# Performance work log

Measured on AMD Instinct MI355X. Metric: run time of the kernel, lower is better.

## Reference

```python
import jax, jax.numpy as jnp
import numpy as np

WINDOW_SIZE = 11
N_CHANNELS = 3
SIGMA = 1.5
K1, K2 = 0.01, 0.03
VALUE_RANGE = 1.0


def _create_window(window_size: int, n_channels: int, sigma: float) -> np.ndarray:
    # 1D gaussian, normalized, then outer product -> 2D kernel
    coords = np.arange(window_size, dtype=np.float32) - (window_size - 1) / 2.0
    g = np.exp(-(coords ** 2) / (2.0 * sigma ** 2))
    g = g / g.sum()
    k2d = np.outer(g, g).astype(np.float32)  # (K, K), sums to 1
    # depthwise kernel, OIHW with I=1 (groups = n_channels)
    return np.broadcast_to(k2d, (n_channels, 1, window_size, window_size)).copy()


def _dwconv(x, window):
    # depthwise valid conv, NCHW / OIHW
    return jax.lax.conv_general_dilated(
        x, window, window_strides=(1, 1), padding='VALID',
        feature_group_count=window.shape[0],
        dimension_numbers=('NCHW', 'OIHW', 'NCHW'))


def setup_inputs() -> dict:
    key = jax.random.key(0)
    kx, ky = jax.random.split(key)
    N, C, H, W = 32, N_CHANNELS, 512, 512
    x = jax.random.uniform(kx, (N, C, H, W), dtype=jnp.float32)
    y = jax.random.uniform(ky, (N, C, H, W), dtype=jnp.float32)
    window = jnp.asarray(_create_window(WINDOW_SIZE, N_CHANNELS, SIGMA))
    return {"x": x, "y": y, "window": window}


def reference(x, y, window):
    c1 = (K1 * VALUE_RANGE) ** 2
    c2 = (K2 * VALUE_RANGE) ** 2

    mu_x = _dwconv(x, window)
    mu_y = _dwconv(y, window)
    mu_x_sq = mu_x ** 2
    mu_y_sq = mu_y ** 2
    mu_xy = mu_x * mu_y

    sigma_x_sq = _dwconv(x * x, window) - mu_x_sq
    sigma_y_sq = _dwconv(y * y, window) - mu_y_sq
    sigma_xy = _dwconv(x * y, window) - mu_xy

    cs = (2.0 * sigma_xy + c2) / (sigma_x_sq + sigma_y_sq + c2)
    ss = (2.0 * mu_xy + c1) / (mu_x_sq + mu_y_sq + c1) * cs

    l = ss.mean(axis=(-1, -2))  # (N, C) per-channel SSIM
    l = l.mean(axis=-1)         # (N,)  per-sample
    return l.mean()             # reduction='mean'
```

## Files before the change

kernel.cpp:

```cpp
#include <hip/hip_runtime.h>

#define KS     11
#define HH     512
#define WW     512
#define OUTD   502
#define OH     45
#define ROWS   55
#define NBANDS 12
#define NSTRIP 4
#define SCOLS  128
#define LCOLS  140
#define NIMG   96
#define NACC   256

__global__ __launch_bounds__(64, 2)
void ssim_main(const float* __restrict__ xg, const float* __restrict__ yg,
               const float* __restrict__ win, double* __restrict__ acc_out,
               const int accmask)
{
    __shared__ float shs[2][LCOLS];
    __shared__ float shd[2][LCOLS];

    const int tid   = threadIdx.x;
    const int bid   = blockIdx.x;
    const int strip = bid & (NSTRIP - 1);
    const int band  = (bid >> 2) % NBANDS;
    const int img   = bid / (NSTRIP * NBANDS);
    const int row0  = band * OH;
    const int colb  = strip * SCOLS;
    const int c0    = colb + 2 * tid;
    const int l0    = 2 * tid;

    float g[6];
    #pragma unroll
    for (int i = 0; i < 6; i++) {
        float s = 0.f;
        #pragma unroll
        for (int j = 0; j < KS; j++) s += win[i * KS + j];
        g[i] = s;
    }
#define G(j) g[(j) <= 5 ? (j) : 10 - (j)]

    const float* xi = xg + (size_t)img * (HH * WW);
    const float* yi = yg + (size_t)img * (HH * WW);

    const bool hn = (tid < (LCOLS - SCOLS) / 2);
    int hcol = colb + SCOLS + 2 * tid;
    if (hcol > WW - 2) hcol = WW - 2;

    float acc[4][2][KS];
    #pragma unroll
    for (int q = 0; q < 4; q++)
        #pragma unroll
        for (int c = 0; c < 2; c++)
            #pragma unroll
            for (int s = 0; s < KS; s++) acc[q][c][s] = 0.f;

    float ssum = 0.f;
    const float C1x2 = 0.0002f;
    const float C2x2 = 0.0018f;

    float2 pfs, pfd, phs, phd;
    {
        int gr = row0;
        float2 ax = *(const float2*)&xi[gr * WW + c0];
        float2 ay = *(const float2*)&yi[gr * WW + c0];
        shs[0][l0] = ax.x + ay.x; shs[0][l0 + 1] = ax.y + ay.y;
        shd[0][l0] = ax.x - ay.x; shd[0][l0 + 1] = ax.y - ay.y;
        if (hn) {
            float2 bx = *(const float2*)&xi[gr * WW + hcol];
            float2 by = *(const float2*)&yi[gr * WW + hcol];
            shs[0][SCOLS + l0] = bx.x + by.x; shs[0][SCOLS + l0 + 1] = bx.y + by.y;
            shd[0][SCOLS + l0] = bx.x - by.x; shd[0][SCOLS + l0 + 1] = bx.y - by.y;
        }
        gr = row0 + 1;
        ax = *(const float2*)&xi[gr * WW + c0];
        ay = *(const float2*)&yi[gr * WW + c0];
        pfs = make_float2(ax.x + ay.x, ax.y + ay.y);
        pfd = make_float2(ax.x - ay.x, ax.y - ay.y);
        phs = make_float2(0.f, 0.f); phd = make_float2(0.f, 0.f);
        if (hn) {
            float2 bx = *(const float2*)&xi[gr * WW + hcol];
            float2 by = *(const float2*)&yi[gr * WW + hcol];
            phs = make_float2(bx.x + by.x, bx.y + by.y);
            phd = make_float2(bx.x - by.x, bx.y - by.y);
        }
    }

    #pragma unroll 1
    for (int rb = 0; rb < ROWS / KS; rb++) {
        #pragma unroll
        for (int rr = 0; rr < KS; rr++) {
            const int r = rb * KS + rr;

            const float* sb = shs[r & 1];
            const float* db = shd[r & 1];
            float sv[12], dv[12];
            #pragma unroll
            for (int k = 0; k < 6; k++) {
                float2 a = *(const float2*)&sb[l0 + 2 * k];
                float2 b = *(const float2*)&db[l0 + 2 * k];
                sv[2 * k] = a.x; sv[2 * k + 1] = a.y;
                dv[2 * k] = b.x; dv[2 * k + 1] = b.y;
            }

            if (r + 1 < ROWS) {
                float* sw = shs[(r + 1) & 1];
                float* dw = shd[(r + 1) & 1];
                sw[l0] = pfs.x; sw[l0 + 1] = pfs.y;
                dw[l0] = pfd.x; dw[l0 + 1] = pfd.y;
                if (hn) {
                    sw[SCOLS + l0] = phs.x; sw[SCOLS + l0 + 1] = phs.y;
                    dw[SCOLS + l0] = phd.x; dw[SCOLS + l0 + 1] = phd.y;
                }
            }
            if (r + 2 < ROWS) {
                int gr = row0 + r + 2; if (gr > HH - 1) gr = HH - 1;
                float2 ax = *(const float2*)&xi[gr * WW + c0];
                float2 ay = *(const float2*)&yi[gr * WW + c0];
                pfs = make_float2(ax.x + ay.x, ax.y + ay.y);
                pfd = make_float2(ax.x - ay.x, ax.y - ay.y);
                if (hn) {
                    float2 bx = *(const float2*)&xi[gr * WW + hcol];
                    float2 by = *(const float2*)&yi[gr * WW + hcol];
                    phs = make_float2(bx.x + by.x, bx.y + by.y);
                    phd = make_float2(bx.x - by.x, bx.y - by.y);
                }
            }

            float h0a = 0.f, h0b = 0.f, h1a = 0.f, h1b = 0.f;
            float h2a = 0.f, h2b = 0.f, h3a = 0.f, h3b = 0.f;
            float ts = sv[0] * sv[0];
            float td = dv[0] * dv[0];
            #pragma unroll
            for (int j = 0; j < KS; j++) {
                const float gj  = G(j);
                const float tsn = sv[j + 1] * sv[j + 1];
                const float tdn = dv[j + 1] * dv[j + 1];
                h0a = fmaf(gj, sv[j],     h0a); h0b = fmaf(gj, sv[j + 1], h0b);
                h1a = fmaf(gj, dv[j],     h1a); h1b = fmaf(gj, dv[j + 1], h1b);
                h2a = fmaf(gj, ts,        h2a); h2b = fmaf(gj, tsn,       h2b);
                h3a = fmaf(gj, td,        h3a); h3b = fmaf(gj, tdn,       h3b);
                ts = tsn; td = tdn;
            }

            {
                const float g0 = G(0);
                acc[0][0][rr] = g0 * h0a; acc[0][1][rr] = g0 * h0b;
                acc[1][0][rr] = g0 * h1a; acc[1][1][rr] = g0 * h1b;
                acc[2][0][rr] = g0 * h2a; acc[2][1][rr] = g0 * h2b;
                acc[3][0][rr] = g0 * h3a; acc[3][1][rr] = g0 * h3b;
            }
            #pragma unroll
            for (int i = 1; i < KS; i++) {
                const int slot = (rr - i + KS) % KS;
                const float gi = G(i);
                acc[0][0][slot] = fmaf(gi, h0a, acc[0][0][slot]);
                acc[0][1][slot] = fmaf(gi, h0b, acc[0][1][slot]);
                acc[1][0][slot] = fmaf(gi, h1a, acc[1][0][slot]);
                acc[1][1][slot] = fmaf(gi, h1b, acc[1][1][slot]);
                acc[2][0][slot] = fmaf(gi, h2a, acc[2][0][slot]);
                acc[2][1][slot] = fmaf(gi, h2b, acc[2][1][slot]);
                acc[3][0][slot] = fmaf(gi, h3a, acc[3][0][slot]);
                acc[3][1][slot] = fmaf(gi, h3b, acc[3][1][slot]);
            }

            const int es   = (rr + 1) % KS;
            const int jloc = r - (KS - 1);
            if (jloc >= 0 && jloc < OH && (row0 + jloc) < OUTD) {
                #pragma unroll
                for (int c = 0; c < 2; c++) {
                    if (c0 + c < OUTD) {
                        const float ms = acc[0][c][es], md = acc[1][c][es];
                        const float Ss = acc[2][c][es], Sd = acc[3][c][es];
                        const float a = ms * ms, b = md * md;
                        const float P = a - b;
                        const float Q = a + b;
                        const float U = Ss - Sd;
                        const float V = Ss + Sd;
                        const float num = (P + C1x2) * ((U - P) + C2x2);
                        const float den = (Q + C1x2) * ((V - Q) + C2x2);
                        float rc = __builtin_amdgcn_rcpf(den);
                        rc = rc * fmaf(-den, rc, 2.0f);
                        ssum = fmaf(num, rc, ssum);
                    }
                }
            }
        }
    }

    #pragma unroll
    for (int off = 32; off > 0; off >>= 1)
        ssum += __shfl_down(ssum, off);
    if (tid == 0)
        atomicAdd(&acc_out[bid & accmask], (double)ssum);
}

__global__ void ssim_finalize(const double* __restrict__ acc, float* __restrict__ out,
                              const int nacc)
{
    double s = 0.0;
    for (int i = threadIdx.x; i < nacc; i += 64) s += acc[i];
    #pragma unroll
    for (int off = 32; off > 0; off >>= 1)
        s += __shfl_down(s, off);
    if (threadIdx.x == 0)
        out[0] = (float)(s * (1.0 / 24192384.0));
}

extern "C" void kernel_launch(void* const* d_in, const int* in_sizes, int n_in,
                              void* d_out, int out_size, void* d_ws, size_t ws_size,
                              hipStream_t stream)
{
    const float* x   = (const float*)d_in[0];
    const float* y   = (const float*)d_in[1];
    const float* win = (const float*)d_in[2];
    float* out = (float*)d_out;
    double* acc = (double*)d_ws;

    const int nacc = (ws_size >= NACC * sizeof(double)) ? NACC : 1;
    hipMemsetAsync(acc, 0, nacc * sizeof(double), stream);
    ssim_main<<<dim3(NIMG * NBANDS * NSTRIP), dim3(64), 0, stream>>>(
        x, y, win, acc, nacc - 1);
    ssim_finalize<<<dim3(1), dim3(64), 0, stream>>>(acc, out, nacc);
}
```

Before: 329.4 us.

## Replace LDS row buffer with wavefront shuffles and interleaved x/y lanes

Each wavefront now covers a 52-column strip. Lanes alternate between loading x and y pairs, and each lane pair builds sum and difference values through xor shuffles. The horizontal 11-tap window is gathered with shuffle-down, so the shared-memory double buffer and its staging stores go away. Bands grow taller (133 output rows), which shrinks the vertical halo overhead, and register state is halved so launch bounds can allow 4 waves per SIMD. The cost is redundant halo columns per strip (64 lanes for 52 outputs), many extra cross-lane shuffles per row, and fewer blocks in total.

```diff
diff --git a/kernel.cpp b/kernel.cpp
--- a/kernel.cpp
+++ b/kernel.cpp
@@ -4,32 +4,26 @@
 #define HH     512
 #define WW     512
 #define OUTD   502
-#define OH     45
-#define ROWS   55
-#define NBANDS 12
-#define NSTRIP 4
-#define SCOLS  128
-#define LCOLS  140
+#define OH     133
+#define ROWS   143
+#define NBANDS 4
+#define ECOLS  52
+#define NSTRIP 10
 #define NIMG   96
 #define NACC   256
 
-__global__ __launch_bounds__(64, 2)
+__global__ __launch_bounds__(64, 4)
 void ssim_main(const float* __restrict__ xg, const float* __restrict__ yg,
                const float* __restrict__ win, double* __restrict__ acc_out,
                const int accmask)
 {
-    __shared__ float shs[2][LCOLS];
-    __shared__ float shd[2][LCOLS];
-
-    const int tid   = threadIdx.x;
-    const int bid   = blockIdx.x;
-    const int strip = bid & (NSTRIP - 1);
-    const int band  = (bid >> 2) % NBANDS;
-    const int img   = bid / (NSTRIP * NBANDS);
-    const int row0  = band * OH;
-    const int colb  = strip * SCOLS;
-    const int c0    = colb + 2 * tid;
-    const int l0    = 2 * tid;
+    const int lane   = threadIdx.x;
+    const int bid    = blockIdx.x;
+    const int strip  = bid % NSTRIP;
+    const int band   = (bid / NSTRIP) % NBANDS;
+    const int img    = bid / (NSTRIP * NBANDS);
+    const int row0   = band * OH;
+    const int parity = lane & 1;
 
     float g[6];
     #pragma unroll
@@ -41,16 +35,14 @@
     }
 #define G(j) g[(j) <= 5 ? (j) : 10 - (j)]
 
-    const float* xi = xg + (size_t)img * (HH * WW);
-    const float* yi = yg + (size_t)img * (HH * WW);
+    int gcol = ECOLS * strip + (lane & ~1);
+    if (gcol > WW - 2) gcol = WW - 2;
+    const float* srcp = (parity ? yg : xg) + (size_t)img * (HH * WW) + gcol;
+    const float sgn = parity ? -1.f : 1.f;
 
-    const bool hn = (tid < (LCOLS - SCOLS) / 2);
-    int hcol = colb + SCOLS + 2 * tid;
-    if (hcol > WW - 2) hcol = WW - 2;
-
-    float acc[4][2][KS];
+    float acc[2][2][KS];
     #pragma unroll
-    for (int q = 0; q < 4; q++)
+    for (int q = 0; q < 2; q++)
         #pragma unroll
         for (int c = 0; c < 2; c++)
             #pragma unroll
@@ -60,32 +52,7 @@
     const float C1x2 = 0.0002f;
     const float C2x2 = 0.0018f;
 
-    float2 pfs, pfd, phs, phd;
-    {
-        int gr = row0;
-        float2 ax = *(const float2*)&xi[gr * WW + c0];
-        float2 ay = *(const float2*)&yi[gr * WW + c0];
-        shs[0][l0] = ax.x + ay.x; shs[0][l0 + 1] = ax.y + ay.y;
-        shd[0][l0] = ax.x - ay.x; shd[0][l0 + 1] = ax.y - ay.y;
-        if (hn) {
-            float2 bx = *(const float2*)&xi[gr * WW + hcol];
-            float2 by = *(const float2*)&yi[gr * WW + hcol];
-            shs[0][SCOLS + l0] = bx.x + by.x; shs[0][SCOLS + l0 + 1] = bx.y + by.y;
-            shd[0][SCOLS + l0] = bx.x - by.x; shd[0][SCOLS + l0 + 1] = bx.y - by.y;
-        }
-        gr = row0 + 1;
-        ax = *(const float2*)&xi[gr * WW + c0];
-        ay = *(const float2*)&yi[gr * WW + c0];
-        pfs = make_float2(ax.x + ay.x, ax.y + ay.y);
-        pfd = make_float2(ax.x - ay.x, ax.y - ay.y);
-        phs = make_float2(0.f, 0.f); phd = make_float2(0.f, 0.f);
-        if (hn) {
-            float2 bx = *(const float2*)&xi[gr * WW + hcol];
-            float2 by = *(const float2*)&yi[gr * WW + hcol];
-            phs = make_float2(bx.x + by.x, bx.y + by.y);
-            phd = make_float2(bx.x - by.x, bx.y - by.y);
-        }
-    }
+    float2 pf = *(const float2*)(srcp + (size_t)row0 * WW);
 
     #pragma unroll 1
     for (int rb = 0; rb < ROWS / KS; rb++) {
@@ -93,98 +60,76 @@
         for (int rr = 0; rr < KS; rr++) {
             const int r = rb * KS + rr;
 
-            const float* sb = shs[r & 1];
-            const float* db = shd[r & 1];
-            float sv[12], dv[12];
-            #pragma unroll
-            for (int k = 0; k < 6; k++) {
-                float2 a = *(const float2*)&sb[l0 + 2 * k];
-                float2 b = *(const float2*)&db[l0 + 2 * k];
-                sv[2 * k] = a.x; sv[2 * k + 1] = a.y;
-                dv[2 * k] = b.x; dv[2 * k + 1] = b.y;
+            const float2 cur = pf;
+            {
+                int gr = row0 + r + 1; if (gr > HH - 1) gr = HH - 1;
+                pf = *(const float2*)(srcp + (size_t)gr * WW);
             }
 
-            if (r + 1 < ROWS) {
-                float* sw = shs[(r + 1) & 1];
-                float* dw = shd[(r + 1) & 1];
-                sw[l0] = pfs.x; sw[l0 + 1] = pfs.y;
-                dw[l0] = pfd.x; dw[l0 + 1] = pfd.y;
-                if (hn) {
-                    sw[SCOLS + l0] = phs.x; sw[SCOLS + l0 + 1] = phs.y;
-                    dw[SCOLS + l0] = phd.x; dw[SCOLS + l0 + 1] = phd.y;
-                }
-            }
-            if (r + 2 < ROWS) {
-                int gr = row0 + r + 2; if (gr > HH - 1) gr = HH - 1;
-                float2 ax = *(const float2*)&xi[gr * WW + c0];
-                float2 ay = *(const float2*)&yi[gr * WW + c0];
-                pfs = make_float2(ax.x + ay.x, ax.y + ay.y);
-                pfd = make_float2(ax.x - ay.x, ax.y - ay.y);
-                if (hn) {
-                    float2 bx = *(const float2*)&xi[gr * WW + hcol];
-                    float2 by = *(const float2*)&yi[gr * WW + hcol];
-                    phs = make_float2(bx.x + by.x, bx.y + by.y);
-                    phd = make_float2(bx.x - by.x, bx.y - by.y);
-                }
+            const float px = __shfl_xor(cur.x, 1);
+            const float py = __shfl_xor(cur.y, 1);
+            const float v0 = fmaf(sgn, cur.x, px);
+            const float v1 = fmaf(sgn, cur.y, py);
+
+            float sv[12];
+            sv[0] = v0; sv[1] = v1;
+            #pragma unroll
+            for (int k = 1; k <= 5; k++) {
+                sv[2 * k]     = __shfl_down(v0, 2 * k);
+                sv[2 * k + 1] = __shfl_down(v1, 2 * k);
             }
 
-            float h0a = 0.f, h0b = 0.f, h1a = 0.f, h1b = 0.f;
-            float h2a = 0.f, h2b = 0.f, h3a = 0.f, h3b = 0.f;
-            float ts = sv[0] * sv[0];
-            float td = dv[0] * dv[0];
+            float hv0 = 0.f, hv1 = 0.f, hq0 = 0.f, hq1 = 0.f;
+            float q0 = sv[0] * sv[0];
             #pragma unroll
             for (int j = 0; j < KS; j++) {
-                const float gj  = G(j);
-                const float tsn = sv[j + 1] * sv[j + 1];
-                const float tdn = dv[j + 1] * dv[j + 1];
-                h0a = fmaf(gj, sv[j],     h0a); h0b = fmaf(gj, sv[j + 1], h0b);
-                h1a = fmaf(gj, dv[j],     h1a); h1b = fmaf(gj, dv[j + 1], h1b);
-                h2a = fmaf(gj, ts,        h2a); h2b = fmaf(gj, tsn,       h2b);
-                h3a = fmaf(gj, td,        h3a); h3b = fmaf(gj, tdn,       h3b);
-                ts = tsn; td = tdn;
+                const float gj = G(j);
+                const float q1 = sv[j + 1] * sv[j + 1];
+                hv0 = fmaf(gj, sv[j],     hv0);
+                hv1 = fmaf(gj, sv[j + 1], hv1);
+                hq0 = fmaf(gj, q0,        hq0);
+                hq1 = fmaf(gj, q1,        hq1);
+                q0 = q1;
             }
 
             {
                 const float g0 = G(0);
-                acc[0][0][rr] = g0 * h0a; acc[0][1][rr] = g0 * h0b;
-                acc[1][0][rr] = g0 * h1a; acc[1][1][rr] = g0 * h1b;
-                acc[2][0][rr] = g0 * h2a; acc[2][1][rr] = g0 * h2b;
-                acc[3][0][rr] = g0 * h3a; acc[3][1][rr] = g0 * h3b;
+                acc[0][0][rr] = g0 * hv0; acc[0][1][rr] = g0 * hv1;
+                acc[1][0][rr] = g0 * hq0; acc[1][1][rr] = g0 * hq1;
             }
             #pragma unroll
             for (int i = 1; i < KS; i++) {
                 const int slot = (rr - i + KS) % KS;
                 const float gi = G(i);
-                acc[0][0][slot] = fmaf(gi, h0a, acc[0][0][slot]);
-                acc[0][1][slot] = fmaf(gi, h0b, acc[0][1][slot]);
-                acc[1][0][slot] = fmaf(gi, h1a, acc[1][0][slot]);
-                acc[1][1][slot] = fmaf(gi, h1b, acc[1][1][slot]);
-                acc[2][0][slot] = fmaf(gi, h2a, acc[2][0][slot]);
-                acc[2][1][slot] = fmaf(gi, h2b, acc[2][1][slot]);
-                acc[3][0][slot] = fmaf(gi, h3a, acc[3][0][slot]);
-                acc[3][1][slot] = fmaf(gi, h3b, acc[3][1][slot]);
+                acc[0][0][slot] = fmaf(gi, hv0, acc[0][0][slot]);
+                acc[0][1][slot] = fmaf(gi, hv1, acc[0][1][slot]);
+                acc[1][0][slot] = fmaf(gi, hq0, acc[1][0][slot]);
+                acc[1][1][slot] = fmaf(gi, hq1, acc[1][1][slot]);
             }
 
             const int es   = (rr + 1) % KS;
             const int jloc = r - (KS - 1);
-            if (jloc >= 0 && jloc < OH && (row0 + jloc) < OUTD) {
-                #pragma unroll
-                for (int c = 0; c < 2; c++) {
-                    if (c0 + c < OUTD) {
-                        const float ms = acc[0][c][es], md = acc[1][c][es];
-                        const float Ss = acc[2][c][es], Sd = acc[3][c][es];
-                        const float a = ms * ms, b = md * md;
-                        const float P = a - b;
-                        const float Q = a + b;
-                        const float U = Ss - Sd;
-                        const float V = Ss + Sd;
-                        const float num = (P + C1x2) * ((U - P) + C2x2);
-                        const float den = (Q + C1x2) * ((V - Q) + C2x2);
-                        float rc = __builtin_amdgcn_rcpf(den);
-                        rc = rc * fmaf(-den, rc, 2.0f);
-                        ssum = fmaf(num, rc, ssum);
-                    }
-                }
+            const int ecol = ECOLS * strip + lane;
+            if (jloc >= 0 && jloc < OH && (row0 + jloc) < OUTD &&
+                lane < ECOLS && ecol < OUTD) {
+                const float pm0 = __shfl_xor(acc[0][0][es], 1);
+                const float pm1 = __shfl_xor(acc[0][1][es], 1);
+                const float pS0 = __shfl_xor(acc[1][0][es], 1);
+                const float pS1 = __shfl_xor(acc[1][1][es], 1);
+                const float ms = parity ? pm1 : acc[0][0][es];
+                const float md = parity ? acc[0][1][es] : pm0;
+                const float Ss = parity ? pS1 : acc[1][0][es];
+                const float Sd = parity ? acc[1][1][es] : pS0;
+                const float a = ms * ms, b = md * md;
+                const float P = a - b;
+                const float Q = a + b;
+                const float U = Ss - Sd;
+                const float V = Ss + Sd;
+                const float num = (P + C1x2) * ((U - P) + C2x2);
+                const float den = (Q + C1x2) * ((V - Q) + C2x2);
+                float rc = __builtin_amdgcn_rcpf(den);
+                rc = rc * fmaf(-den, rc, 2.0f);
+                ssum = fmaf(num, rc, ssum);
             }
         }
     }
@@ -192,7 +137,7 @@
     #pragma unroll
     for (int off = 32; off > 0; off >>= 1)
         ssum += __shfl_down(ssum, off);
-    if (tid == 0)
+    if (lane == 0)
         atomicAdd(&acc_out[bid & accmask], (double)ssum);
 }
 
```

Measured after the change: 274.1 us. 16.8% less time.

## Load overlapping row windows directly from global memory instead of via LDS, taller bands

Applied to the files above, without the earlier changes.

Each lane now loads its own 12-column window of x and y straight from global memory, six float2 loads per input per row, and keeps the sums and differences in registers. This drops the shared-memory double buffer and its writes and reads. Band height grows from 45 to 67 output rows, with 8 bands instead of 12, which cuts the fraction of halo rows that get recomputed. In exchange, each lane issues six times as many global/L1 loads per row, grid size drops by a third, and register pressure rises from the larger prefetch arrays.

```diff
diff --git a/kernel.cpp b/kernel.cpp
--- a/kernel.cpp
+++ b/kernel.cpp
@@ -4,12 +4,11 @@
 #define HH     512
 #define WW     512
 #define OUTD   502
-#define OH     45
-#define ROWS   55
-#define NBANDS 12
+#define OH     67
+#define ROWS   77
+#define NBANDS 8
+#define SCOLS  128
 #define NSTRIP 4
-#define SCOLS  128
-#define LCOLS  140
 #define NIMG   96
 #define NACC   256
 
@@ -18,18 +17,13 @@
                const float* __restrict__ win, double* __restrict__ acc_out,
                const int accmask)
 {
-    __shared__ float shs[2][LCOLS];
-    __shared__ float shd[2][LCOLS];
-
-    const int tid   = threadIdx.x;
+    const int lane  = threadIdx.x;
     const int bid   = blockIdx.x;
     const int strip = bid & (NSTRIP - 1);
     const int band  = (bid >> 2) % NBANDS;
     const int img   = bid / (NSTRIP * NBANDS);
     const int row0  = band * OH;
-    const int colb  = strip * SCOLS;
-    const int c0    = colb + 2 * tid;
-    const int l0    = 2 * tid;
+    const int bc    = strip * SCOLS + 2 * lane;
 
     float g[6];
     #pragma unroll
@@ -41,12 +35,15 @@
     }
 #define G(j) g[(j) <= 5 ? (j) : 10 - (j)]
 
+    int coff[6];
+    #pragma unroll
+    for (int k = 0; k < 6; k++) {
+        int c = bc + 2 * k;
+        coff[k] = (c > WW - 2) ? (WW - 2) : c;
+    }
+
     const float* xi = xg + (size_t)img * (HH * WW);
     const float* yi = yg + (size_t)img * (HH * WW);
-
-    const bool hn = (tid < (LCOLS - SCOLS) / 2);
-    int hcol = colb + SCOLS + 2 * tid;
-    if (hcol > WW - 2) hcol = WW - 2;
 
     float acc[4][2][KS];
     #pragma unroll
@@ -60,30 +57,25 @@
     const float C1x2 = 0.0002f;
     const float C2x2 = 0.0018f;
 
-    float2 pfs, pfd, phs, phd;
+    float sv[12], dv[12];
+    float2 lx[6], ly[6];
+
     {
-        int gr = row0;
-        float2 ax = *(const float2*)&xi[gr * WW + c0];
-        float2 ay = *(const float2*)&yi[gr * WW + c0];
-        shs[0][l0] = ax.x + ay.x; shs[0][l0 + 1] = ax.y + ay.y;
-        shd[0][l0] = ax.x - ay.x; shd[0][l0 + 1] = ax.y - ay.y;
-        if (hn) {
-            float2 bx = *(const float2*)&xi[gr * WW + hcol];
-            float2 by = *(const float2*)&yi[gr * WW + hcol];
-            shs[0][SCOLS + l0] = bx.x + by.x; shs[0][SCOLS + l0 + 1] = bx.y + by.y;
-            shd[0][SCOLS + l0] = bx.x - by.x; shd[0][SCOLS + l0 + 1] = bx.y - by.y;
+        const float* xr = xi + (size_t)row0 * WW;
+        const float* yr = yi + (size_t)row0 * WW;
+        #pragma unroll
+        for (int k = 0; k < 6; k++) {
+            float2 a = *(const float2*)(xr + coff[k]);
+            float2 b = *(const float2*)(yr + coff[k]);
+            sv[2 * k] = a.x + b.x; sv[2 * k + 1] = a.y + b.y;
+            dv[2 * k] = a.x - b.x; dv[2 * k + 1] = a.y - b.y;
         }
-        gr = row0 + 1;
-        ax = *(const float2*)&xi[gr * WW + c0];
-        ay = *(const float2*)&yi[gr * WW + c0];
-        pfs = make_float2(ax.x + ay.x, ax.y + ay.y);
-        pfd = make_float2(ax.x - ay.x, ax.y - ay.y);
-        phs = make_float2(0.f, 0.f); phd = make_float2(0.f, 0.f);
-        if (hn) {
-            float2 bx = *(const float2*)&xi[gr * WW + hcol];
-            float2 by = *(const float2*)&yi[gr * WW + hcol];
-            phs = make_float2(bx.x + by.x, bx.y + by.y);
-            phd = make_float2(bx.x - by.x, bx.y - by.y);
+        const float* xr1 = xi + (size_t)(row0 + 1) * WW;
+        const float* yr1 = yi + (size_t)(row0 + 1) * WW;
+        #pragma unroll
+        for (int k = 0; k < 6; k++) {
+            lx[k] = *(const float2*)(xr1 + coff[k]);
+            ly[k] = *(const float2*)(yr1 + coff[k]);
         }
     }
 
@@ -93,76 +85,41 @@
         for (int rr = 0; rr < KS; rr++) {
             const int r = rb * KS + rr;
 
-            const float* sb = shs[r & 1];
-            const float* db = shd[r & 1];
-            float sv[12], dv[12];
-            #pragma unroll
-            for (int k = 0; k < 6; k++) {
-                float2 a = *(const float2*)&sb[l0 + 2 * k];
-                float2 b = *(const float2*)&db[l0 + 2 * k];
-                sv[2 * k] = a.x; sv[2 * k + 1] = a.y;
-                dv[2 * k] = b.x; dv[2 * k + 1] = b.y;
-            }
-
-            if (r + 1 < ROWS) {
-                float* sw = shs[(r + 1) & 1];
-                float* dw = shd[(r + 1) & 1];
-                sw[l0] = pfs.x; sw[l0 + 1] = pfs.y;
-                dw[l0] = pfd.x; dw[l0 + 1] = pfd.y;
-                if (hn) {
-                    sw[SCOLS + l0] = phs.x; sw[SCOLS + l0 + 1] = phs.y;
-                    dw[SCOLS + l0] = phd.x; dw[SCOLS + l0 + 1] = phd.y;
-                }
-            }
-            if (r + 2 < ROWS) {
-                int gr = row0 + r + 2; if (gr > HH - 1) gr = HH - 1;
-                float2 ax = *(const float2*)&xi[gr * WW + c0];
-                float2 ay = *(const float2*)&yi[gr * WW + c0];
-                pfs = make_float2(ax.x + ay.x, ax.y + ay.y);
-                pfd = make_float2(ax.x - ay.x, ax.y - ay.y);
-                if (hn) {
-                    float2 bx = *(const float2*)&xi[gr * WW + hcol];
-                    float2 by = *(const float2*)&yi[gr * WW + hcol];
-                    phs = make_float2(bx.x + by.x, bx.y + by.y);
-                    phd = make_float2(bx.x - by.x, bx.y - by.y);
-                }
-            }
-
-            float h0a = 0.f, h0b = 0.f, h1a = 0.f, h1b = 0.f;
-            float h2a = 0.f, h2b = 0.f, h3a = 0.f, h3b = 0.f;
-            float ts = sv[0] * sv[0];
-            float td = dv[0] * dv[0];
+            float hs0 = 0.f, hs1 = 0.f, hd0 = 0.f, hd1 = 0.f;
+            float hS0 = 0.f, hS1 = 0.f, hD0 = 0.f, hD1 = 0.f;
+            float qs = sv[0] * sv[0];
+            float qd = dv[0] * dv[0];
             #pragma unroll
             for (int j = 0; j < KS; j++) {
                 const float gj  = G(j);
-                const float tsn = sv[j + 1] * sv[j + 1];
-                const float tdn = dv[j + 1] * dv[j + 1];
-                h0a = fmaf(gj, sv[j],     h0a); h0b = fmaf(gj, sv[j + 1], h0b);
-                h1a = fmaf(gj, dv[j],     h1a); h1b = fmaf(gj, dv[j + 1], h1b);
-                h2a = fmaf(gj, ts,        h2a); h2b = fmaf(gj, tsn,       h2b);
-                h3a = fmaf(gj, td,        h3a); h3b = fmaf(gj, tdn,       h3b);
-                ts = tsn; td = tdn;
+                const float qs1 = sv[j + 1] * sv[j + 1];
+                const float qd1 = dv[j + 1] * dv[j + 1];
+                hs0 = fmaf(gj, sv[j],     hs0);  hs1 = fmaf(gj, sv[j + 1], hs1);
+                hd0 = fmaf(gj, dv[j],     hd0);  hd1 = fmaf(gj, dv[j + 1], hd1);
+                hS0 = fmaf(gj, qs,        hS0);  hS1 = fmaf(gj, qs1,       hS1);
+                hD0 = fmaf(gj, qd,        hD0);  hD1 = fmaf(gj, qd1,       hD1);
+                qs = qs1; qd = qd1;
             }
 
             {
                 const float g0 = G(0);
-                acc[0][0][rr] = g0 * h0a; acc[0][1][rr] = g0 * h0b;
-                acc[1][0][rr] = g0 * h1a; acc[1][1][rr] = g0 * h1b;
-                acc[2][0][rr] = g0 * h2a; acc[2][1][rr] = g0 * h2b;
-                acc[3][0][rr] = g0 * h3a; acc[3][1][rr] = g0 * h3b;
+                acc[0][0][rr] = g0 * hs0; acc[0][1][rr] = g0 * hs1;
+                acc[1][0][rr] = g0 * hd0; acc[1][1][rr] = g0 * hd1;
+                acc[2][0][rr] = g0 * hS0; acc[2][1][rr] = g0 * hS1;
+                acc[3][0][rr] = g0 * hD0; acc[3][1][rr] = g0 * hD1;
             }
             #pragma unroll
             for (int i = 1; i < KS; i++) {
                 const int slot = (rr - i + KS) % KS;
                 const float gi = G(i);
-                acc[0][0][slot] = fmaf(gi, h0a, acc[0][0][slot]);
-                acc[0][1][slot] = fmaf(gi, h0b, acc[0][1][slot]);
-                acc[1][0][slot] = fmaf(gi, h1a, acc[1][0][slot]);
-                acc[1][1][slot] = fmaf(gi, h1b, acc[1][1][slot]);
-                acc[2][0][slot] = fmaf(gi, h2a, acc[2][0][slot]);
-                acc[2][1][slot] = fmaf(gi, h2b, acc[2][1][slot]);
-                acc[3][0][slot] = fmaf(gi, h3a, acc[3][0][slot]);
-                acc[3][1][slot] = fmaf(gi, h3b, acc[3][1][slot]);
+                acc[0][0][slot] = fmaf(gi, hs0, acc[0][0][slot]);
+                acc[0][1][slot] = fmaf(gi, hs1, acc[0][1][slot]);
+                acc[1][0][slot] = fmaf(gi, hd0, acc[1][0][slot]);
+                acc[1][1][slot] = fmaf(gi, hd1, acc[1][1][slot]);
+                acc[2][0][slot] = fmaf(gi, hS0, acc[2][0][slot]);
+                acc[2][1][slot] = fmaf(gi, hS1, acc[2][1][slot]);
+                acc[3][0][slot] = fmaf(gi, hD0, acc[3][0][slot]);
+                acc[3][1][slot] = fmaf(gi, hD1, acc[3][1][slot]);
             }
 
             const int es   = (rr + 1) % KS;
@@ -170,7 +127,7 @@
             if (jloc >= 0 && jloc < OH && (row0 + jloc) < OUTD) {
                 #pragma unroll
                 for (int c = 0; c < 2; c++) {
-                    if (c0 + c < OUTD) {
+                    if (bc + c < OUTD) {
                         const float ms = acc[0][c][es], md = acc[1][c][es];
                         const float Ss = acc[2][c][es], Sd = acc[3][c][es];
                         const float a = ms * ms, b = md * md;
@@ -186,13 +143,33 @@
                     }
                 }
             }
+
+            if (r + 1 < ROWS) {
+                #pragma unroll
+                for (int k = 0; k < 6; k++) {
+                    sv[2 * k]     = lx[k].x + ly[k].x;
+                    sv[2 * k + 1] = lx[k].y + ly[k].y;
+                    dv[2 * k]     = lx[k].x - ly[k].x;
+                    dv[2 * k + 1] = lx[k].y - ly[k].y;
+                }
+            }
+            if (r + 2 < ROWS) {
+                int gr = row0 + r + 2; if (gr > HH - 1) gr = HH - 1;
+                const float* xr = xi + (size_t)gr * WW;
+                const float* yr = yi + (size_t)gr * WW;
+                #pragma unroll
+                for (int k = 0; k < 6; k++) {
+                    lx[k] = *(const float2*)(xr + coff[k]);
+                    ly[k] = *(const float2*)(yr + coff[k]);
+                }
+            }
         }
     }
 
     #pragma unroll
     for (int off = 32; off > 0; off >>= 1)
         ssum += __shfl_down(ssum, off);
-    if (tid == 0)
+    if (lane == 0)
         atomicAdd(&acc_out[bid & accmask], (double)ssum);
 }
 
```

Result: faster. 308.3 us (-6.4%).
